# Performance work log

Measured on AMD Instinct MI355X. Metric: run time of the kernel, lower is better.

Reference implementation:

```python
import jax, jax.numpy as jnp
import numpy as np

B, S, A = 64, 256, 256
V, P, TE, PE, AE, H, L = 50000, 48, 256, 64, 64, 512, 24
WD = TE + PE          # word_dim = token_embed + pos_embed
NA = 3 * L + 3        # Shift + L Unary + 2L Reduce/Reduce* + Pad + Pop


def setup_inputs() -> dict:
    key = jax.random.key(0)
    ks = jax.random.split(key, 24)
    f = lambda i, shape: jax.random.normal(ks[i], shape, dtype=jnp.float32) * 0.05
    return dict(
        token_batch=jax.random.randint(ks[0], (B, S), 0, V),
        pos_batch=jax.random.randint(ks[1], (B, S), 0, P),
        label_batch=jax.random.randint(ks[2], (B, S), 0, L),
        action_batch=jax.random.randint(ks[3], (B, A), 0, NA - 2),  # exclude Pad/Pop
        word_emb=f(4, (V, TE)), pos_emb=f(5, (P, PE)), action_emb=f(6, (NA, AE)),
        tok_Wih=f(7, (4 * H, WD)), tok_Whh=f(8, (4 * H, H)), tok_b=f(9, (4 * H,)),
        st_Wih=f(10, (4 * H, H)), st_Whh=f(11, (4 * H, H)), st_b=f(12, (4 * H,)),
        ac_Wih=f(13, (4 * H, AE)), ac_Whh=f(14, (4 * H, H)), ac_b=f(15, (4 * H,)),
        red_W=f(16, (2 * L, WD, 2 * WD)), red_b=f(17, (2 * L, WD)),
        comp_W=f(18, (H, WD)), comp_b=f(19, (H,)),
        h2f_W=f(20, (H, 5 * H)), h2f_b=f(21, (H,)),
        f2a_W=f(22, (NA, H)), f2a_b=f(23, (NA,)),
    )


def _lstm_cell(x, h, c, Wih, Whh, b):
    g = x @ Wih.T + h @ Whh.T + b
    i, fg, gg, o = jnp.split(g, 4, axis=-1)
    c = jax.nn.sigmoid(fg) * c + jax.nn.sigmoid(i) * jnp.tanh(gg)
    return jax.nn.sigmoid(o) * jnp.tanh(c), c


def reference(token_batch, pos_batch, label_batch, action_batch,
              word_emb, pos_emb, action_emb,
              tok_Wih, tok_Whh, tok_b,
              st_Wih, st_Whh, st_b,
              ac_Wih, ac_Whh, ac_b,
              red_W, red_b, comp_W, comp_b,
              h2f_W, h2f_b, f2a_W, f2a_b):
    # token encoder: embed + concat + unidirectional LSTM over the sentence
    tok = jnp.concatenate([word_emb[token_batch], pos_emb[pos_batch]], -1)  # [B,S,WD]

    def tstep(carry, x):
        h, c = carry
        h, c = _lstm_cell(x, h, c, tok_Wih, tok_Whh, tok_b)
        return (h, c), h

    h0 = jnp.zeros((B, H), tok.dtype)
    (_, _), tok_out = jax.lax.scan(tstep, (h0, h0), jnp.swapaxes(tok, 0, 1))  # [S,B,H]

    # action-step scan: action LSTMCell + per-label tiny linear composition +
    # stack LSTMCell + 5H decision feature -> hidden2feat -> relu -> feat2act
    a_emb = action_emb[action_batch]                      # [B,A,AE]
    labels = action_batch % (2 * L)                        # per-step label selection
    tok_prev = jnp.concatenate([tok[:, :1], tok[:, :-1]], 1)
    pair = jnp.concatenate([tok[:, :A], tok_prev[:, :A]], -1)  # [B,A,2WD]

    def astep(carry, x):
        ha, ca, hs, cs, h1 = carry
        ae_t, lab_t, pair_t, buf_t, act_t = x
        ha, ca = _lstm_cell(ae_t, ha, ca, ac_Wih, ac_Whh, ac_b)
        # per-label reduce linear (2*WD -> WD), gathered by the step's label
        composed = jnp.tanh(jnp.einsum('bij,bj->bi', red_W[lab_t], pair_t) + red_b[lab_t])
        st_in = buf_t + composed @ comp_W.T + comp_b
        hs_new, cs = _lstm_cell(st_in, hs, cs, st_Wih, st_Whh, st_b)
        feat = jnp.concatenate([hs_new, hs, h1, buf_t, ha], -1)  # [B,5H]
        logits = jax.nn.relu(feat @ h2f_W.T + h2f_b) @ f2a_W.T + f2a_b
        logp = jax.nn.log_softmax(logits, -1)
        loss_t = -jnp.take_along_axis(logp, act_t[:, None], 1)[:, 0]
        return (ha, ca, hs_new, cs, hs), loss_t

    z = jnp.zeros((B, H), tok.dtype)
    xs = (jnp.swapaxes(a_emb, 0, 1), labels.T, jnp.swapaxes(pair, 0, 1),
          tok_out[:A], action_batch.T)
    _, losses = jax.lax.scan(astep, (z, z, z, z, z), xs)  # [A,B]
    return jnp.mean(losses)
```

## Files before the change

kernel.cpp:

```cpp
#include <hip/hip_runtime.h>
#include <math.h>

constexpr int nB = 64, nS = 256, nAc = 256, nH = 512, nG = 2048;
constexpr int nWD = 320, nNA = 75, nLB = 48, nFH = 2560;
constexpr int BH = nB * nH;

typedef _Float16 h16;
typedef _Float16 h16x8 __attribute__((ext_vector_type(8)));
typedef _Float16 h16x4 __attribute__((ext_vector_type(4)));
typedef _Float16 h16x2 __attribute__((ext_vector_type(2)));
typedef float f32x4 __attribute__((ext_vector_type(4)));
typedef unsigned long long u64t;

__device__ __forceinline__ float sigf(float x) { return 1.0f / (1.0f + __expf(-x)); }

#if __has_builtin(__builtin_amdgcn_fdot2)
#define FDOT2(a, b, c) __builtin_amdgcn_fdot2((a), (b), (c), false)
#else
__device__ __forceinline__ float FDOT2(h16x2 a, h16x2 b, float c) {
    return c + (float)a[0] * (float)b[0] + (float)a[1] * (float)b[1];
}
#endif

__global__ void init_k(h16* __restrict__ hsrec, int* __restrict__ counts, int* __restrict__ fill,
                       u64t* __restrict__ hbuf, u64t* __restrict__ spbuf, u64t* __restrict__ apbuf)
{
    int i = blockIdx.x * 256 + threadIdx.x;
    if (i < 2 * BH) hsrec[i] = (h16)0.0f;
    if (i < 32768) { hbuf[i] = 0; spbuf[i] = 0; apbuf[i] = 0; }
    if (i < nLB) { counts[i] = 0; fill[i] = 0; }
}

__global__ __launch_bounds__(256)
void cvt_k(const float* __restrict__ src, h16* __restrict__ dst, int n4)
{
    const int i = blockIdx.x * 256 + threadIdx.x;
    if (i < n4) {
        const float4 a = ((const float4*)src)[i];
        h16x4 v; v[0]=(h16)a.x; v[1]=(h16)a.y; v[2]=(h16)a.z; v[3]=(h16)a.w;
        ((h16x4*)dst)[i] = v;
    }
}

__global__ __launch_bounds__(64)
void embed_k(const int* __restrict__ tokb, const int* __restrict__ posb,
             const float* __restrict__ wemb, const float* __restrict__ pemb,
             h16* __restrict__ tok)
{
    const int r = blockIdx.x;
    const int tid = threadIdx.x;
    const int tk = tokb[r], pp = posb[r];
    h16x8* d = (h16x8*)(tok + (size_t)r * nWD);
    if (tid < 32) {
        const float4* sw = (const float4*)(wemb + (size_t)tk * 256);
        const float4 a = sw[2 * tid], b = sw[2 * tid + 1];
        h16x8 o;
        o[0]=(h16)a.x; o[1]=(h16)a.y; o[2]=(h16)a.z; o[3]=(h16)a.w;
        o[4]=(h16)b.x; o[5]=(h16)b.y; o[6]=(h16)b.z; o[7]=(h16)b.w;
        d[tid] = o;
    } else if (tid < 40) {
        const int q = tid - 32;
        const float4* sp = (const float4*)(pemb + (size_t)pp * 64);
        const float4 a = sp[2 * q], b = sp[2 * q + 1];
        h16x8 o;
        o[0]=(h16)a.x; o[1]=(h16)a.y; o[2]=(h16)a.z; o[3]=(h16)a.w;
        o[4]=(h16)b.x; o[5]=(h16)b.y; o[6]=(h16)b.z; o[7]=(h16)b.w;
        d[32 + q] = o;
    }
}

__global__ __launch_bounds__(256)
void actab_k(const float* __restrict__ aemb, const float* __restrict__ aWih,
             const float* __restrict__ ab, float* __restrict__ acTab)
{
    const int a = blockIdx.x;
    __shared__ float ae[64];
    const int tid = threadIdx.x;
    if (tid < 64) ae[tid] = aemb[a * 64 + tid];
    __syncthreads();
    for (int j = tid; j < nG; j += 256) {
        const float* wr = aWih + (size_t)j * 64;
        float s = ab[j];
        #pragma unroll
        for (int k = 0; k < 64; k += 4) {
            const float4 w = *(const float4*)(wr + k);
            s = fmaf(w.x, ae[k], s);     s = fmaf(w.y, ae[k + 1], s);
            s = fmaf(w.z, ae[k + 2], s); s = fmaf(w.w, ae[k + 3], s);
        }
        acTab[(size_t)a * nG + j] = s;
    }
}

template<int MODE, bool RELU>
__global__ __launch_bounds__(256)
void mgemm_k(const h16* __restrict__ Wm, const float* __restrict__ bias,
             const h16* __restrict__ A0, const h16* __restrict__ A1,
             const h16* __restrict__ A2, h16* __restrict__ C, int Ktot, int ldC)
{
    const int bm = blockIdx.x << 6, bn = blockIdx.y << 6;
    const int tid = threadIdx.x;
    const int lane = tid & 63, wave = tid >> 6;
    const int wr = wave >> 1, wc = wave & 1;
    __shared__ __align__(16) h16 As[64][40];
    __shared__ __align__(16) h16 Ws[64][40];
    const int srow = tid >> 2, sk = (tid & 3) << 3;
    const int r3 = bm + srow;
    const h16* arow = nullptr;
    if (MODE == 0) { const int b = r3 & 63, s = r3 >> 6; arow = A0 + ((size_t)b * nS + s) * nWD; }
    if (MODE == 5) { arow = A0 + (size_t)r3 * nWD; }
    const h16* wrow = Wm + (size_t)(bn + srow) * Ktot;
    f32x4 acc[2][2] = {};
    for (int k0 = 0; k0 < Ktot; k0 += 32) {
        h16x8 av, wv;
        if (MODE == 3) {
            const int k = k0 + sk;
            const int p = k >> 9;
            const h16* base = (p == 0) ? A0 + 2 * BH : (p == 1) ? A0 + BH
                            : (p == 2) ? A0 : (p == 3) ? A1 : A2;
            av = *(const h16x8*)(base + (size_t)r3 * nH + (k & 511));
        } else {
            av = *(const h16x8*)(arow + k0 + sk);
        }
        wv = *(const h16x8*)(wrow + k0 + sk);
        __syncthreads();
        *(h16x8*)(&As[srow][sk]) = av;
        *(h16x8*)(&Ws[srow][sk]) = wv;
        __syncthreads();
        const int fk = (lane >> 4) << 3;
        const int fr = lane & 15;
        h16x8 af0 = *(const h16x8*)(&As[(wr << 5) + fr][fk]);
        h16x8 af1 = *(const h16x8*)(&As[(wr << 5) + 16 + fr][fk]);
        h16x8 bf0 = *(const h16x8*)(&Ws[(wc << 5) + fr][fk]);
        h16x8 bf1 = *(const h16x8*)(&Ws[(wc << 5) + 16 + fr][fk]);
        acc[0][0] = __builtin_amdgcn_mfma_f32_16x16x32_f16(af0, bf0, acc[0][0], 0, 0, 0);
        acc[0][1] = __builtin_amdgcn_mfma_f32_16x16x32_f16(af0, bf1, acc[0][1], 0, 0, 0);
        acc[1][0] = __builtin_amdgcn_mfma_f32_16x16x32_f16(af1, bf0, acc[1][0], 0, 0, 0);
        acc[1][1] = __builtin_amdgcn_mfma_f32_16x16x32_f16(af1, bf1, acc[1][1], 0, 0, 0);
    }
    #pragma unroll
    for (int mi = 0; mi < 2; ++mi) {
        #pragma unroll
        for (int ni = 0; ni < 2; ++ni) {
            const int col = bn + (wc << 5) + (ni << 4) + (lane & 15);
            const float bs = bias[col];
            #pragma unroll
            for (int rg = 0; rg < 4; ++rg) {
                const int row = bm + (wr << 5) + (mi << 4) + ((lane >> 4) << 2) + rg;
                float x = acc[mi][ni][rg] + bs;
                if (RELU) x = fmaxf(x, 0.0f);
                C[(size_t)row * ldC + col] = (h16)x;
            }
        }
    }
}

__global__ void hist_k(const int* __restrict__ actb, int* __restrict__ lab, int* __restrict__ counts)
{
    const int r = blockIdx.x * 256 + threadIdx.x;
    const int t = r >> 6, b = r & 63;
    const int a = actb[b * nAc + t];
    const int l = a % nLB;
    lab[r] = l;
    atomicAdd(&counts[l], 1);
}

__global__ void tiles_k(const int* __restrict__ counts, int* __restrict__ offs,
                        int* __restrict__ tl_lab, int* __restrict__ tl_start,
                        int* __restrict__ tl_cnt, int* __restrict__ ntiles)
{
    if (blockIdx.x == 0 && threadIdx.x == 0) {
        int o = 0, nt = 0;
        for (int l = 0; l < nLB; ++l) {
            offs[l] = o;
            const int c = counts[l];
            for (int s0 = 0; s0 < c; s0 += 64) {
                tl_lab[nt] = l; tl_start[nt] = o + s0; tl_cnt[nt] = min(64, c - s0); ++nt;
            }
            o += c;
        }
        offs[nLB] = o;
        ntiles[0] = nt;
    }
}

__global__ void scatter_k(const int* __restrict__ lab, const int* __restrict__ offs,
                          int* __restrict__ fill, int* __restrict__ idx)
{
    const int r = blockIdx.x * 256 + threadIdx.x;
    const int l = lab[r];
    const int pos = offs[l] + atomicAdd(&fill[l], 1);
    idx[pos] = r;
}

__global__ __launch_bounds__(256)
void comp_gemm_k(const h16* __restrict__ tok, const float* __restrict__ redW,
                 const float* __restrict__ redb, const int* __restrict__ idx,
                 const int* __restrict__ tl_lab, const int* __restrict__ tl_start,
                 const int* __restrict__ tl_cnt, const int* __restrict__ ntiles,
                 h16* __restrict__ comp)
{
    const int tile = blockIdx.x;
    if (tile >= ntiles[0]) return;
    const int cn0 = blockIdx.y << 6;
    const int l = tl_lab[tile], rst = tl_start[tile], mrows = tl_cnt[tile];
    __shared__ int rows_s[64];
    __shared__ __align__(16) float As[16][68];
    __shared__ __align__(16) float Ws[16][68];
    const int tid = threadIdx.x;
    if (tid < 64) rows_s[tid] = (tid < mrows) ? idx[rst + tid] : -1;
    __syncthreads();
    const int alm = tid >> 1, alk = (tid & 1) << 3;
    const int wlm = tid >> 2, wlk = (tid & 3) << 2;
    const int trow = tid >> 4, tcol = tid & 15;
    const int rm = (tid < 128) ? rows_s[alm] : -1;
    const h16* arow0 = tok;
    const h16* arow1 = tok;
    if (rm >= 0) {
        const int b = rm & 63, t = rm >> 6;
        arow0 = tok + ((size_t)b * nS + t) * nWD;
        arow1 = tok + ((size_t)b * nS + max(t - 1, 0)) * nWD;
    }
    const float* wrow = redW + (size_t)l * (320 * 640) + (size_t)(cn0 + wlm) * 640;
    float acc[4][4] = {};
    for (int k0 = 0; k0 < 640; k0 += 16) {
        const int k = k0 + alk;
        h16x8 av = {};
        if (rm >= 0) av = (k < 320) ? *(const h16x8*)(arow0 + k)
                                    : *(const h16x8*)(arow1 + (k - 320));
        const float4 wv = *(const float4*)(wrow + k0 + wlk);
        __syncthreads();
        if (tid < 128) {
            #pragma unroll
            for (int j = 0; j < 8; ++j) As[alk + j][alm] = (float)av[j];
        }
        Ws[wlk + 0][wlm] = wv.x; Ws[wlk + 1][wlm] = wv.y;
        Ws[wlk + 2][wlm] = wv.z; Ws[wlk + 3][wlm] = wv.w;
        __syncthreads();
        #pragma unroll
        for (int kk = 0; kk < 16; ++kk) {
            const float4 a4 = *(const float4*)&As[kk][trow << 2];
            const float4 w4 = *(const float4*)&Ws[kk][tcol << 2];
            const float aa[4] = {a4.x, a4.y, a4.z, a4.w};
            const float ww[4] = {w4.x, w4.y, w4.z, w4.w};
            #pragma unroll
            for (int i = 0; i < 4; ++i)
                #pragma unroll
                for (int j = 0; j < 4; ++j)
                    acc[i][j] = fmaf(aa[i], ww[j], acc[i][j]);
        }
    }
    #pragma unroll
    for (int i = 0; i < 4; ++i) {
        const int rr = rows_s[(trow << 2) + i];
        if (rr < 0) continue;
        #pragma unroll
        for (int j = 0; j < 4; ++j) {
            const int cc = cn0 + (tcol << 2) + j;
            comp[(size_t)rr * nWD + cc] = (h16)tanhf(acc[i][j] + redb[l * nWD + cc]);
        }
    }
}

__global__ __launch_bounds__(512, 4)
void fused_scan_k(const h16* __restrict__ tW16, const h16* __restrict__ sWhh16,
                  const h16* __restrict__ sWih16, const h16* __restrict__ aW16,
                  const h16* __restrict__ gxTok, const float* __restrict__ acTab,
                  const int* __restrict__ actb, const h16* __restrict__ P1h,
                  const float* __restrict__ sbias,
                  u64t* __restrict__ hq_tok, u64t* __restrict__ hq_st, u64t* __restrict__ hq_ac,
                  h16* __restrict__ tokrec, h16* __restrict__ hsrec, h16* __restrict__ harec)
{
    __shared__ __align__(16) h16 hsmS[8][nH];
    __shared__ __align__(16) h16 hsmT[8][nH];
    __shared__ float psF[8192];
    __shared__ float gexF[1152];
    __shared__ int aidx[8];
    const int blk = blockIdx.x;
    const int tid = threadIdx.x;

    if (blk < 256) {
        const int role = blk >> 7;
        const int sub = blk & 127;
        const int g = sub >> 4, jb = sub & 15;
        const int kg = tid >> 6;
        const int rp = tid & 63;
        const int r0 = rp << 1;
        const int grow0 = (r0 >> 5) * nH + (jb << 5) + (r0 & 31);
        const int rr = tid & 127;
        const int bq = tid >> 7;
        const int growR = (rr >> 5) * nH + (jb << 5) + (rr & 31);
        const h16* W = role ? aW16 : tW16;
        u64t* hq = role ? hq_ac : hq_tok;
        h16x8 w0[8], w1[8];
        {
            const h16* wp0 = W + (size_t)grow0 * nH + (kg << 6);
            const h16* wp1 = wp0 + nH;
            #pragma unroll
            for (int i = 0; i < 8; ++i) {
                w0[i] = *(const h16x8*)(wp0 + (i << 3));
                w1[i] = *(const h16x8*)(wp1 + (i << 3));
            }
        }
        float creg[2] = {0.0f, 0.0f};
        const size_t gbase = (size_t)g << 11;
        for (int t = 0; t < nS; ++t) {
            float gp[2];
            if (role == 0) {
                #pragma unroll
                for (int u = 0; u < 2; ++u)
                    gp[u] = (float)gxTok[(size_t)((t << 6) + (g << 3) + (bq << 1) + u) * nG + growR];
            } else if (tid < 8) {
                aidx[tid] = actb[((g << 3) + tid) * nAc + t];
            }
            if (t == 0) {
                ((uint4*)hsmS)[tid] = make_uint4(0u, 0u, 0u, 0u);
            } else {
                const int want = t;
                u64t* base = hq + (size_t)((t - 1) & 1) * 16384 + gbase;
                u64t v[4];
                #pragma unroll
                for (int i = 0; i < 4; ++i)
                    v[i] = __hip_atomic_load(base + tid + (i << 9), __ATOMIC_RELAXED, __HIP_MEMORY_SCOPE_AGENT);
                #pragma unroll
                for (int i = 0; i < 4; ++i) {
                    while ((int)(v[i] >> 32) != want) {
                        __builtin_amdgcn_s_sleep(1);
                        v[i] = __hip_atomic_load(base + tid + (i << 9), __ATOMIC_RELAXED, __HIP_MEMORY_SCOPE_AGENT);
                    }
                    ((unsigned*)hsmS)[tid + (i << 9)] = (unsigned)v[i];
                }
            }
            __syncthreads();
            if (role == 1) {
                #pragma unroll
                for (int u = 0; u < 2; ++u)
                    gp[u] = acTab[(size_t)aidx[(bq << 1) + u] * nG + growR];
            }
            float acc0[8] = {0,0,0,0,0,0,0,0}, acc1[8] = {0,0,0,0,0,0,0,0};
            #pragma unroll
            for (int i = 0; i < 8; ++i) {
                const h16x2* wa = (const h16x2*)&w0[i];
                const h16x2* wb = (const h16x2*)&w1[i];
                #pragma unroll
                for (int b = 0; b < 8; ++b) {
                    h16x8 hv = *(const h16x8*)(&hsmS[b][(kg << 6) + (i << 3)]);
                    const h16x2* hp = (const h16x2*)&hv;
                    acc0[b] = FDOT2(hp[0], wa[0], acc0[b]);
                    acc0[b] = FDOT2(hp[1], wa[1], acc0[b]);
                    acc0[b] = FDOT2(hp[2], wa[2], acc0[b]);
                    acc0[b] = FDOT2(hp[3], wa[3], acc0[b]);
                    acc1[b] = FDOT2(hp[0], wb[0], acc1[b]);
                    acc1[b] = FDOT2(hp[1], wb[1], acc1[b]);
                    acc1[b] = FDOT2(hp[2], wb[2], acc1[b]);
                    acc1[b] = FDOT2(hp[3], wb[3], acc1[b]);
                }
            }
            #pragma unroll
            for (int b = 0; b < 8; ++b) {
                float2 pv; pv.x = acc0[b]; pv.y = acc1[b];
                *(float2*)&psF[(((kg << 3) + b) << 7) + r0] = pv;
            }
            __syncthreads();
            #pragma unroll
            for (int u = 0; u < 2; ++u) {
                const int b = (bq << 1) + u;
                float s = gp[u];
                #pragma unroll
                for (int k2 = 0; k2 < 8; ++k2) s += psF[(((k2 << 3) + b) << 7) + rr];
                gexF[rr * 9 + b] = s;
            }
            if (role == 0 && t >= 2 && tid == 0) {
                u64t* fp = hq_st + (size_t)(t & 1) * 16384 + gbase;
                u64t v = __hip_atomic_load(fp, __ATOMIC_RELAXED, __HIP_MEMORY_SCOPE_AGENT);
                while ((int)(v >> 32) < t - 1) {
                    __builtin_amdgcn_s_sleep(1);
                    v = __hip_atomic_load(fp, __ATOMIC_RELAXED, __HIP_MEMORY_SCOPE_AGENT);
                }
            }
            __syncthreads();
            if (tid < 128) {
                const int q = tid >> 3, b2 = tid & 7;
                const int jl0 = q << 1;
                float hn[2];
                #pragma unroll
                for (int u = 0; u < 2; ++u) {
                    const int j = jl0 + u;
                    const float gi = gexF[j * 9 + b2], gf = gexF[(32 + j) * 9 + b2];
                    const float gg = gexF[(64 + j) * 9 + b2], go = gexF[(96 + j) * 9 + b2];
                    const float cn = sigf(gf) * creg[u] + sigf(gi) * tanhf(gg);
                    hn[u] = sigf(go) * tanhf(cn);
                    creg[u] = cn;
                }
                const int bg = (g << 3) + b2;
                h16x2 hp2; hp2[0] = (h16)hn[0]; hp2[1] = (h16)hn[1];
                const u64t word = ((u64t)(unsigned)(t + 1) << 32) | __builtin_bit_cast(unsigned, hp2);
                __hip_atomic_store(hq + (size_t)(t & 1) * 16384 + ((size_t)bg << 8) + (jb << 4) + q,
                                   word, __ATOMIC_RELAXED, __HIP_MEMORY_SCOPE_AGENT);
                h16* rec = role ? (harec + (size_t)t * BH) : (tokrec + (size_t)t * BH);
                *(h16x2*)(rec + (size_t)bg * nH + (jb << 5) + jl0) = hp2;
            }
        }
    } else {
        const int sub = blk - 256;
        const int g = sub >> 5, jb = sub & 31;
        const int kg = tid >> 5;
        const int rp = tid & 31;
        const int r0 = rp << 1;
        const int grow0 = (r0 >> 4) * nH + (jb << 4) + (r0 & 15);
        const int rr = tid & 63, bR = tid >> 6;
        const int growR = (rr >> 4) * nH + (jb << 4) + (rr & 15);
        h16x8 wa0[4], wa1[4], wb0[4], wb1[4];
        {
            const h16* a0p = sWhh16 + (size_t)grow0 * nH + (kg << 5);
            const h16* b0p = sWih16 + (size_t)grow0 * nH + (kg << 5);
            #pragma unroll
            for (int i = 0; i < 4; ++i) {
                wa0[i] = *(const h16x8*)(a0p + (i << 3));
                wa1[i] = *(const h16x8*)(a0p + nH + (i << 3));
                wb0[i] = *(const h16x8*)(b0p + (i << 3));
                wb1[i] = *(const h16x8*)(b0p + nH + (i << 3));
            }
        }
        const float gbias = sbias[growR];
        float creg[2] = {0.0f, 0.0f};
        const size_t gbase = (size_t)g << 11;
        for (int t = 0; t < nAc; ++t) {
            if (t == 0) {
                ((uint4*)hsmS)[tid] = make_uint4(0u, 0u, 0u, 0u);
            } else {
                const int want = t;
                u64t* base = hq_st + (size_t)((t - 1) & 1) * 16384 + gbase;
                u64t v[4];
                #pragma unroll
                for (int i = 0; i < 4; ++i)
                    v[i] = __hip_atomic_load(base + tid + (i << 9), __ATOMIC_RELAXED, __HIP_MEMORY_SCOPE_AGENT);
                #pragma unroll
                for (int i = 0; i < 4; ++i) {
                    while ((int)(v[i] >> 32) != want) {
                        __builtin_amdgcn_s_sleep(1);
                        v[i] = __hip_atomic_load(base + tid + (i << 9), __ATOMIC_RELAXED, __HIP_MEMORY_SCOPE_AGENT);
                    }
                    ((unsigned*)hsmS)[tid + (i << 9)] = (unsigned)v[i];
                }
            }
            {
                const int want = t + 1;
                u64t* base = hq_tok + (size_t)(t & 1) * 16384 + gbase;
                const unsigned* p1p = (const unsigned*)(P1h + (size_t)t * BH) + (g << 11);
                u64t v[4];
                #pragma unroll
                for (int i = 0; i < 4; ++i)
                    v[i] = __hip_atomic_load(base + tid + (i << 9), __ATOMIC_RELAXED, __HIP_MEMORY_SCOPE_AGENT);
                #pragma unroll
                for (int i = 0; i < 4; ++i) {
                    while ((int)(v[i] >> 32) != want) {
                        __builtin_amdgcn_s_sleep(1);
                        v[i] = __hip_atomic_load(base + tid + (i << 9), __ATOMIC_RELAXED, __HIP_MEMORY_SCOPE_AGENT);
                    }
                    const h16x2 tv = __builtin_bit_cast(h16x2, (unsigned)v[i]);
                    const h16x2 pv = __builtin_bit_cast(h16x2, p1p[tid + (i << 9)]);
                    h16x2 sum; sum[0] = tv[0] + pv[0]; sum[1] = tv[1] + pv[1];
                    ((unsigned*)hsmT)[tid + (i << 9)] = __builtin_bit_cast(unsigned, sum);
                }
            }
            __syncthreads();
            float acc0[8] = {0,0,0,0,0,0,0,0}, acc1[8] = {0,0,0,0,0,0,0,0};
            #pragma unroll
            for (int i = 0; i < 4; ++i) {
                const h16x2* pa0 = (const h16x2*)&wa0[i];
                const h16x2* pa1 = (const h16x2*)&wa1[i];
                const h16x2* pb0 = (const h16x2*)&wb0[i];
                const h16x2* pb1 = (const h16x2*)&wb1[i];
                #pragma unroll
                for (int b = 0; b < 8; ++b) {
                    h16x8 hs = *(const h16x8*)(&hsmS[b][(kg << 5) + (i << 3)]);
                    h16x8 ht = *(const h16x8*)(&hsmT[b][(kg << 5) + (i << 3)]);
                    const h16x2* hps = (const h16x2*)&hs;
                    const h16x2* hpt = (const h16x2*)&ht;
                    #pragma unroll
                    for (int p = 0; p < 4; ++p) {
                        acc0[b] = FDOT2(hps[p], pa0[p], acc0[b]);
                        acc0[b] = FDOT2(hpt[p], pb0[p], acc0[b]);
                        acc1[b] = FDOT2(hps[p], pa1[p], acc1[b]);
                        acc1[b] = FDOT2(hpt[p], pb1[p], acc1[b]);
                    }
                }
            }
            #pragma unroll
            for (int b = 0; b < 8; ++b) {
                float2 pv; pv.x = acc0[b]; pv.y = acc1[b];
                *(float2*)&psF[(((kg << 3) + b) << 6) + r0] = pv;
            }
            __syncthreads();
            {
                float s = gbias;
                #pragma unroll
                for (int k2 = 0; k2 < 16; ++k2) s += psF[(((k2 << 3) + bR) << 6) + rr];
                gexF[rr * 9 + bR] = s;
            }
            __syncthreads();
            if (tid < 64) {
                const int q = tid >> 3, b2 = tid & 7;
                const int jl0 = q << 1;
                float hn[2];
                #pragma unroll
                for (int u = 0; u < 2; ++u) {
                    const int j = jl0 + u;
                    const float gi = gexF[j * 9 + b2], gf = gexF[(16 + j) * 9 + b2];
                    const float gg = gexF[(32 + j) * 9 + b2], go = gexF[(48 + j) * 9 + b2];
                    const float cn = sigf(gf) * creg[u] + sigf(gi) * tanhf(gg);
                    hn[u] = sigf(go) * tanhf(cn);
                    creg[u] = cn;
                }
                const int bg = (g << 3) + b2;
                h16x2 hp2; hp2[0] = (h16)hn[0]; hp2[1] = (h16)hn[1];
                const u64t word = ((u64t)(unsigned)(t + 1) << 32) | __builtin_bit_cast(unsigned, hp2);
                __hip_atomic_store(hq_st + (size_t)(t & 1) * 16384 + ((size_t)bg << 8) + (jb << 3) + q,
                                   word, __ATOMIC_RELAXED, __HIP_MEMORY_SCOPE_AGENT);
                *(h16x2*)(hsrec + (size_t)(t + 2) * BH + (size_t)bg * nH + (jb << 4) + jl0) = hp2;
            }
        }
    }
}

__global__ __launch_bounds__(128)
void loss_k(const h16* __restrict__ hidden, const float* __restrict__ f2aW,
            const float* __restrict__ f2ab, const int* __restrict__ actb,
            float* __restrict__ losses)
{
    const int r = blockIdx.x;
    const int t = r >> 6, b = r & 63;
    __shared__ __align__(16) float hrow[nH];
    __shared__ float lg[nNA + 1];
    const int tid = threadIdx.x;
    if (tid < 64) {
        const h16x8 v = ((const h16x8*)(hidden + (size_t)r * nH))[tid];
        #pragma unroll
        for (int j = 0; j < 8; ++j) hrow[tid * 8 + j] = (float)v[j];
    }
    __syncthreads();
    if (tid < nNA) {
        const float* wr = f2aW + (size_t)tid * nH;
        float a = f2ab[tid];
        for (int k = 0; k < nH; k += 4) {
            const float4 wv = *(const float4*)(wr + k);
            const float4 hv = *(const float4*)(&hrow[k]);
            a = fmaf(wv.x, hv.x, a); a = fmaf(wv.y, hv.y, a);
            a = fmaf(wv.z, hv.z, a); a = fmaf(wv.w, hv.w, a);
        }
        lg[tid] = a;
    }
    __syncthreads();
    if (tid < 64) {
        float m = -1e30f;
        for (int i = tid; i < nNA; i += 64) m = fmaxf(m, lg[i]);
        #pragma unroll
        for (int o = 32; o > 0; o >>= 1) m = fmaxf(m, __shfl_xor(m, o));
        float s = 0.0f;
        for (int i = tid; i < nNA; i += 64) s += __expf(lg[i] - m);
        #pragma unroll
        for (int o = 32; o > 0; o >>= 1) s += __shfl_xor(s, o);
        if (tid == 0) {
            const int a = actb[b * nAc + t];
            losses[r] = m + logf(s) - lg[a];
        }
    }
}

__global__ __launch_bounds__(256)
void reduce_k(const float* __restrict__ losses, float* __restrict__ out)
{
    __shared__ float sm[256];
    const int tid = threadIdx.x;
    float a = 0.0f;
    for (int i = tid; i < nS * nB; i += 256) a += losses[i];
    sm[tid] = a; __syncthreads();
    for (int s = 128; s > 0; s >>= 1) { if (tid < s) sm[tid] += sm[tid + s]; __syncthreads(); }
    if (tid == 0) out[0] = sm[0] * (1.0f / 16384.0f);
}

extern "C" void kernel_launch(void* const* d_in, const int* in_sizes, int n_in,
                              void* d_out, int out_size, void* d_ws, size_t ws_size,
                              hipStream_t stream)
{
    const int*   tokb  = (const int*)  d_in[0];
    const int*   posb  = (const int*)  d_in[1];
    const int*   actb  = (const int*)  d_in[3];
    const float* wemb  = (const float*)d_in[4];
    const float* pemb  = (const float*)d_in[5];
    const float* aemb  = (const float*)d_in[6];
    const float* tWih  = (const float*)d_in[7];
    const float* tWhh  = (const float*)d_in[8];
    const float* tb    = (const float*)d_in[9];
    const float* sWih  = (const float*)d_in[10];
    const float* sWhh  = (const float*)d_in[11];
    const float* sb    = (const float*)d_in[12];
    const float* aWih  = (const float*)d_in[13];
    const float* aWhh  = (const float*)d_in[14];
    const float* ab    = (const float*)d_in[15];
    const float* redW  = (const float*)d_in[16];
    const float* redb  = (const float*)d_in[17];
    const float* compW = (const float*)d_in[18];
    const float* compb = (const float*)d_in[19];
    const float* h2fW  = (const float*)d_in[20];
    const float* h2fb  = (const float*)d_in[21];
    const float* f2aW  = (const float*)d_in[22];
    const float* f2ab  = (const float*)d_in[23];

    char* base = (char*)d_ws;
    auto carve = [&](size_t bytes) { char* p = base; base += (bytes + 255) & ~(size_t)255; return p; };
    h16*   tok    = (h16*)  carve((size_t)nB * nS * nWD * 2);
    h16*   Xh     = (h16*)  carve((size_t)nS * nB * nG * 2);
    h16*   comph  = (h16*)  carve((size_t)nS * nB * nWD * 2);
    h16*   P1h    = (h16*)  carve((size_t)nS * BH * 2);
    h16*   tokrec = (h16*)  carve((size_t)nS * BH * 2);
    h16*   hsrec  = (h16*)  carve((size_t)(nS + 2) * BH * 2);
    h16*   harec  = (h16*)  carve((size_t)nS * BH * 2);
    h16*   tW16   = (h16*)  carve((size_t)nG * nH * 2);
    h16*   sW16   = (h16*)  carve((size_t)nG * nH * 2);
    h16*   aW16   = (h16*)  carve((size_t)nG * nH * 2);
    h16*   tWih16 = (h16*)  carve((size_t)nG * nWD * 2);
    h16*   sWih16 = (h16*)  carve((size_t)nG * nH * 2);
    h16*   h2f16  = (h16*)  carve((size_t)nH * nFH * 2);
    h16*   comp16 = (h16*)  carve((size_t)nH * nWD * 2);
    float* acTab  = (float*)carve((size_t)nNA * nG * 4);
    u64t*  hbuf   = (u64t*) carve((size_t)2 * 16384 * 8);
    u64t*  spbuf  = (u64t*) carve((size_t)2 * 16384 * 8);
    u64t*  apbuf  = (u64t*) carve((size_t)2 * 16384 * 8);
    float* losses = (float*)carve((size_t)nS * nB * 4);
    int*   lab      = (int*)carve((size_t)nS * nB * 4);
    int*   counts   = (int*)carve(nLB * 4);
    int*   offs     = (int*)carve((nLB + 1) * 4);
    int*   fill     = (int*)carve(nLB * 4);
    int*   tl_lab   = (int*)carve(320 * 4);
    int*   tl_start = (int*)carve(320 * 4);
    int*   tl_cnt   = (int*)carve(320 * 4);
    int*   ntiles   = (int*)carve(4);
    int*   idxb     = (int*)carve((size_t)nS * nB * 4);

    init_k<<<dim3(256), dim3(256), 0, stream>>>(hsrec, counts, fill, hbuf, spbuf, apbuf);
    embed_k<<<dim3(nB * nS), dim3(64), 0, stream>>>(tokb, posb, wemb, pemb, tok);
    actab_k<<<dim3(nNA), dim3(256), 0, stream>>>(aemb, aWih, ab, acTab);
    cvt_k<<<dim3(1024), dim3(256), 0, stream>>>(tWhh, tW16, 262144);
    cvt_k<<<dim3(1024), dim3(256), 0, stream>>>(sWhh, sW16, 262144);
    cvt_k<<<dim3(1024), dim3(256), 0, stream>>>(aWhh, aW16, 262144);
    cvt_k<<<dim3(640),  dim3(256), 0, stream>>>(tWih, tWih16, 163840);
    cvt_k<<<dim3(1024), dim3(256), 0, stream>>>(sWih, sWih16, 262144);
    cvt_k<<<dim3(1280), dim3(256), 0, stream>>>(h2fW, h2f16, 327680);
    cvt_k<<<dim3(160),  dim3(256), 0, stream>>>(compW, comp16, 40960);
    mgemm_k<0,false><<<dim3(256, 32), dim3(256), 0, stream>>>(tWih16, tb, tok, nullptr, nullptr, Xh, nWD, nG);
    hist_k<<<dim3(64), dim3(256), 0, stream>>>(actb, lab, counts);
    tiles_k<<<dim3(1), dim3(64), 0, stream>>>(counts, offs, tl_lab, tl_start, tl_cnt, ntiles);
    scatter_k<<<dim3(64), dim3(256), 0, stream>>>(lab, offs, fill, idxb);
    comp_gemm_k<<<dim3(304, 5), dim3(256), 0, stream>>>(tok, redW, redb, idxb, tl_lab, tl_start, tl_cnt, ntiles, comph);
    mgemm_k<5,false><<<dim3(256, 8), dim3(256), 0, stream>>>(comp16, compb, comph, nullptr, nullptr, P1h, nWD, nH);
    {
        const h16* a0 = tW16; const h16* a1 = sW16; const h16* a2 = sWih16; const h16* a3 = aW16;
        const h16* a4 = Xh; const float* a5 = acTab; const int* a6 = actb;
        const h16* a7 = P1h; const float* a8 = sb;
        u64t* a9 = hbuf; u64t* a10 = spbuf; u64t* a11 = apbuf;
        h16* a12 = tokrec; h16* a13 = hsrec; h16* a14 = harec;
        void* args[] = {&a0, &a1, &a2, &a3, &a4, &a5, &a6, &a7, &a8, &a9, &a10, &a11, &a12, &a13, &a14};
        hipLaunchCooperativeKernel((const void*)fused_scan_k, dim3(512), dim3(512), args, 0, stream);
    }
    mgemm_k<3,true><<<dim3(256, 8), dim3(256), 0, stream>>>(h2f16, h2fb, hsrec, tokrec, harec, Xh, nFH, nH);
    loss_k<<<dim3(nS * nB), dim3(128), 0, stream>>>(Xh, f2aW, f2ab, actb, losses);
    reduce_k<<<dim3(1), dim3(256), 0, stream>>>(losses, (float*)d_out);
}
```

Before: 3.235 ms.

## Decouple token-LSTM from stack-LSTM via 4-deep token hidden ring and add priority hints

Adds a separate 4-slot ring buffer that carries the token LSTM hidden states for the stack-LSTM consumer. This lets the token producer run up to three steps ahead instead of one before it waits on the stack role's progress. It also pins the weight registers with empty asm constraints so the compiler keeps them resident, and raises wave priority around the dot-product loops. The cost is extra global atomic stores per step and a larger init footprint. The init kernel now writes tsbuf unconditionally for all 65536 thread indices, which exactly covers the buffer.

```diff
diff --git a/kernel.cpp b/kernel.cpp
--- a/kernel.cpp
+++ b/kernel.cpp
@@ -22,12 +22,16 @@
 }
 #endif
 
+#define PINV(x) asm volatile("" : "+v"(x))
+
 __global__ void init_k(h16* __restrict__ hsrec, int* __restrict__ counts, int* __restrict__ fill,
-                       u64t* __restrict__ hbuf, u64t* __restrict__ spbuf, u64t* __restrict__ apbuf)
+                       u64t* __restrict__ hbuf, u64t* __restrict__ spbuf, u64t* __restrict__ apbuf,
+                       u64t* __restrict__ tsbuf)
 {
     int i = blockIdx.x * 256 + threadIdx.x;
     if (i < 2 * BH) hsrec[i] = (h16)0.0f;
     if (i < 32768) { hbuf[i] = 0; spbuf[i] = 0; apbuf[i] = 0; }
+    tsbuf[i] = 0;
     if (i < nLB) { counts[i] = 0; fill[i] = 0; }
 }
 
@@ -268,6 +272,7 @@
                   const int* __restrict__ actb, const h16* __restrict__ P1h,
                   const float* __restrict__ sbias,
                   u64t* __restrict__ hq_tok, u64t* __restrict__ hq_st, u64t* __restrict__ hq_ac,
+                  u64t* __restrict__ hq_ts,
                   h16* __restrict__ tokrec, h16* __restrict__ hsrec, h16* __restrict__ harec)
 {
     __shared__ __align__(16) h16 hsmS[8][nH];
@@ -300,6 +305,8 @@
                 w0[i] = *(const h16x8*)(wp0 + (i << 3));
                 w1[i] = *(const h16x8*)(wp1 + (i << 3));
             }
+            #pragma unroll
+            for (int i = 0; i < 8; ++i) { PINV(w0[i]); PINV(w1[i]); }
         }
         float creg[2] = {0.0f, 0.0f};
         const size_t gbase = (size_t)g << 11;
@@ -336,6 +343,7 @@
                 for (int u = 0; u < 2; ++u)
                     gp[u] = acTab[(size_t)aidx[(bq << 1) + u] * nG + growR];
             }
+            __builtin_amdgcn_s_setprio(1);
             float acc0[8] = {0,0,0,0,0,0,0,0}, acc1[8] = {0,0,0,0,0,0,0,0};
             #pragma unroll
             for (int i = 0; i < 8; ++i) {
@@ -355,6 +363,7 @@
                     acc1[b] = FDOT2(hp[3], wb[3], acc1[b]);
                 }
             }
+            __builtin_amdgcn_s_setprio(0);
             #pragma unroll
             for (int b = 0; b < 8; ++b) {
                 float2 pv; pv.x = acc0[b]; pv.y = acc1[b];
@@ -369,10 +378,10 @@
                 for (int k2 = 0; k2 < 8; ++k2) s += psF[(((k2 << 3) + b) << 7) + rr];
                 gexF[rr * 9 + b] = s;
             }
-            if (role == 0 && t >= 2 && tid == 0) {
+            if (role == 0 && t >= 4 && tid == 0) {
                 u64t* fp = hq_st + (size_t)(t & 1) * 16384 + gbase;
                 u64t v = __hip_atomic_load(fp, __ATOMIC_RELAXED, __HIP_MEMORY_SCOPE_AGENT);
-                while ((int)(v >> 32) < t - 1) {
+                while ((int)(v >> 32) < t - 3) {
                     __builtin_amdgcn_s_sleep(1);
                     v = __hip_atomic_load(fp, __ATOMIC_RELAXED, __HIP_MEMORY_SCOPE_AGENT);
                 }
@@ -394,8 +403,13 @@
                 const int bg = (g << 3) + b2;
                 h16x2 hp2; hp2[0] = (h16)hn[0]; hp2[1] = (h16)hn[1];
                 const u64t word = ((u64t)(unsigned)(t + 1) << 32) | __builtin_bit_cast(unsigned, hp2);
-                __hip_atomic_store(hq + (size_t)(t & 1) * 16384 + ((size_t)bg << 8) + (jb << 4) + q,
+                const size_t woff = ((size_t)bg << 8) + (jb << 4) + q;
+                __hip_atomic_store(hq + (size_t)(t & 1) * 16384 + woff,
                                    word, __ATOMIC_RELAXED, __HIP_MEMORY_SCOPE_AGENT);
+                if (role == 0) {
+                    __hip_atomic_store(hq_ts + (size_t)(t & 3) * 16384 + woff,
+                                       word, __ATOMIC_RELAXED, __HIP_MEMORY_SCOPE_AGENT);
+                }
                 h16* rec = role ? (harec + (size_t)t * BH) : (tokrec + (size_t)t * BH);
                 *(h16x2*)(rec + (size_t)bg * nH + (jb << 5) + jl0) = hp2;
             }
@@ -420,6 +434,8 @@
                 wb0[i] = *(const h16x8*)(b0p + (i << 3));
                 wb1[i] = *(const h16x8*)(b0p + nH + (i << 3));
             }
+            #pragma unroll
+            for (int i = 0; i < 4; ++i) { PINV(wa0[i]); PINV(wa1[i]); PINV(wb0[i]); PINV(wb1[i]); }
         }
         const float gbias = sbias[growR];
         float creg[2] = {0.0f, 0.0f};
@@ -445,7 +461,7 @@
             }
             {
                 const int want = t + 1;
-                u64t* base = hq_tok + (size_t)(t & 1) * 16384 + gbase;
+                u64t* base = hq_ts + (size_t)(t & 3) * 16384 + gbase;
                 const unsigned* p1p = (const unsigned*)(P1h + (size_t)t * BH) + (g << 11);
                 u64t v[4];
                 #pragma unroll
@@ -464,6 +480,7 @@
                 }
             }
             __syncthreads();
+            __builtin_amdgcn_s_setprio(1);
             float acc0[8] = {0,0,0,0,0,0,0,0}, acc1[8] = {0,0,0,0,0,0,0,0};
             #pragma unroll
             for (int i = 0; i < 4; ++i) {
@@ -486,6 +503,7 @@
                     }
                 }
             }
+            __builtin_amdgcn_s_setprio(0);
             #pragma unroll
             for (int b = 0; b < 8; ++b) {
                 float2 pv; pv.x = acc0[b]; pv.y = acc1[b];
@@ -627,6 +645,7 @@
     u64t*  hbuf   = (u64t*) carve((size_t)2 * 16384 * 8);
     u64t*  spbuf  = (u64t*) carve((size_t)2 * 16384 * 8);
     u64t*  apbuf  = (u64t*) carve((size_t)2 * 16384 * 8);
+    u64t*  tsbuf  = (u64t*) carve((size_t)4 * 16384 * 8);
     float* losses = (float*)carve((size_t)nS * nB * 4);
     int*   lab      = (int*)carve((size_t)nS * nB * 4);
     int*   counts   = (int*)carve(nLB * 4);
@@ -638,7 +657,7 @@
     int*   ntiles   = (int*)carve(4);
     int*   idxb     = (int*)carve((size_t)nS * nB * 4);
 
-    init_k<<<dim3(256), dim3(256), 0, stream>>>(hsrec, counts, fill, hbuf, spbuf, apbuf);
+    init_k<<<dim3(256), dim3(256), 0, stream>>>(hsrec, counts, fill, hbuf, spbuf, apbuf, tsbuf);
     embed_k<<<dim3(nB * nS), dim3(64), 0, stream>>>(tokb, posb, wemb, pemb, tok);
     actab_k<<<dim3(nNA), dim3(256), 0, stream>>>(aemb, aWih, ab, acTab);
     cvt_k<<<dim3(1024), dim3(256), 0, stream>>>(tWhh, tW16, 262144);
@@ -658,9 +677,9 @@
         const h16* a0 = tW16; const h16* a1 = sW16; const h16* a2 = sWih16; const h16* a3 = aW16;
         const h16* a4 = Xh; const float* a5 = acTab; const int* a6 = actb;
         const h16* a7 = P1h; const float* a8 = sb;
-        u64t* a9 = hbuf; u64t* a10 = spbuf; u64t* a11 = apbuf;
-        h16* a12 = tokrec; h16* a13 = hsrec; h16* a14 = harec;
-        void* args[] = {&a0, &a1, &a2, &a3, &a4, &a5, &a6, &a7, &a8, &a9, &a10, &a11, &a12, &a13, &a14};
+        u64t* a9 = hbuf; u64t* a10 = spbuf; u64t* a11 = apbuf; u64t* a12 = tsbuf;
+        h16* a13 = tokrec; h16* a14 = hsrec; h16* a15 = harec;
+        void* args[] = {&a0, &a1, &a2, &a3, &a4, &a5, &a6, &a7, &a8, &a9, &a10, &a11, &a12, &a13, &a14, &a15};
         hipLaunchCooperativeKernel((const void*)fused_scan_k, dim3(512), dim3(512), args, 0, stream);
     }
     mgemm_k<3,true><<<dim3(256, 8), dim3(256), 0, stream>>>(h2f16, h2fb, hsrec, tokrec, harec, Xh, nFH, nH);
```

Measured after the change: 3.066 ms. 1.06x faster.
